# Kernel tuning notes

Measured on AMD Instinct MI355X. Metric: run time of the kernel, lower is better.

The kernel has to match this reference:

```python
import jax, jax.numpy as jnp
import numpy as np

B, L, IN, OUT = 32, 2048, 192, 2
H, N2, NL = 512, 32, 4  # hidden_dim, d_state//2 complex modes, num_layers


def setup_inputs() -> dict:
    key = jax.random.key(0)
    ks = jax.random.split(key, 8)
    neural_input = jax.random.normal(ks[0], (B, L, IN), jnp.float32)
    W_in = jax.random.normal(ks[1], (IN, H), jnp.float32) / np.sqrt(IN)
    b_in = jnp.zeros((H,), jnp.float32)
    # S4D kernel params (stacked over layers)
    log_dt = jax.random.uniform(ks[2], (NL, H), jnp.float32, np.log(1e-3), np.log(1e-1))
    Cri = jax.random.normal(ks[3], (NL, H, N2, 2), jnp.float32)  # complex C as (re, im)
    log_A_real = jnp.full((NL, H, N2), np.log(0.5), jnp.float32)
    A_imag = jnp.broadcast_to(np.pi * jnp.arange(N2, dtype=np.float32), (NL, H, N2)).astype(jnp.float32)
    D = jax.random.normal(ks[4], (NL, H), jnp.float32)
    # position-wise output conv1x1 producing 2H channels for GLU
    conv_w = jax.random.normal(ks[5], (NL, 2 * H, H), jnp.float32) / np.sqrt(H)
    conv_b = jnp.zeros((NL, 2 * H), jnp.float32)
    W_out = jax.random.normal(ks[6], (H, OUT), jnp.float32) / np.sqrt(H)
    b_out = jnp.zeros((OUT,), jnp.float32)
    return dict(neural_input=neural_input, W_in=W_in, b_in=b_in, log_dt=log_dt,
                Cri=Cri, log_A_real=log_A_real, A_imag=A_imag, D=D,
                conv_w=conv_w, conv_b=conv_b, W_out=W_out, b_out=b_out)


def _s4d_layer(u, log_dt, Cri, log_A_real, A_imag, D, conv_w, conv_b):
    # u: (B, H, L)
    Lx = u.shape[-1]
    dt = jnp.exp(log_dt)[:, None]                       # (H, 1)
    C = Cri[..., 0] + 1j * Cri[..., 1]                  # (H, N2) complex
    A = -jnp.exp(log_A_real) + 1j * A_imag              # (H, N2)
    dtA = A * dt                                        # (H, N2)
    Ct = C * (jnp.exp(dtA) - 1.0) / A                   # (H, N2)
    # Vandermonde kernel: K[h, l] = 2 Re sum_n Ct[h,n] exp(dtA[h,n] * l)
    vand = jnp.exp(dtA[..., None] * jnp.arange(Lx))     # (H, N2, L) complex
    K = 2.0 * jnp.einsum('hn,hnl->hl', Ct, vand).real   # (H, L)
    # circular conv via FFT at length 2L (== linear conv, causal)
    k_f = jnp.fft.rfft(K, n=2 * Lx)
    u_f = jnp.fft.rfft(u, n=2 * Lx)
    y = jnp.fft.irfft(u_f * k_f, n=2 * Lx)[..., :Lx]    # (B, H, L)
    y = y + u * D[:, None]
    y = jax.nn.gelu(y, approximate=False)               # torch nn.GELU (erf)
    # conv1x1 to 2H channels + GLU over channel dim
    z = jnp.einsum('oh,bhl->bol', conv_w, y) + conv_b[None, :, None]
    a, b = jnp.split(z, 2, axis=1)
    return a * jax.nn.sigmoid(b)


def reference(neural_input, W_in, b_in, log_dt, Cri, log_A_real, A_imag, D,
              conv_w, conv_b, W_out, b_out):
    x = neural_input @ W_in + b_in          # (B, L, H)
    u = jnp.transpose(x, (0, 2, 1))         # (B, H, L) channels-first for SSM
    for i in range(NL):
        u = _s4d_layer(u, log_dt[i], Cri[i], log_A_real[i], A_imag[i],
                       D[i], conv_w[i], conv_b[i])
    y = jnp.transpose(u, (0, 2, 1))         # (B, L, H)
    return y @ W_out + b_out                # (B, L, OUT)
```

## Files before the change

kernel.cpp:

```cpp
#include <hip/hip_runtime.h>
#include <hip/hip_bf16.h>
#include <math.h>

#define BB 32
#define LL 2048
#define INP 192
#define OUTC 2
#define HH 512
#define NN2 32
#define NNL 4
#define TABB 32768

using short8 = __attribute__((ext_vector_type(8))) short;
using f32x4  = __attribute__((ext_vector_type(4))) float;
using f32x2  = __attribute__((ext_vector_type(2))) float;

__device__ __forceinline__ float sigmoidf_(float x) {
  return 1.0f / (1.0f + expf(-x));
}
__device__ __forceinline__ unsigned short bf16bits(float x) {
  __hip_bfloat16 b = __float2bfloat16(x);
  return __builtin_bit_cast(unsigned short, b);
}
__device__ __forceinline__ float bfval(unsigned short b) {
  unsigned int u = (unsigned int)b << 16;
  return __builtin_bit_cast(float, u);
}
__device__ __forceinline__ float gelu_fast(float x) {
  float s = x * 0.70710678118654752f;
  float ax = fabsf(s);
  float tt = 1.0f / fmaf(0.3275911f, ax, 1.0f);
  float p = fmaf(1.061405429f, tt, -1.453152027f);
  p = fmaf(p, tt, 1.421413741f);
  p = fmaf(p, tt, -0.284496736f);
  p = fmaf(p, tt, 0.254829592f);
  float e = __expf(-s * s);
  float er = 1.0f - p * tt * e;
  er = copysignf(er, s);
  return 0.5f * x * (1.0f + er);
}
__device__ __forceinline__ void gload16(const void* gsrc, void* ldst) {
  __builtin_amdgcn_global_load_lds(
      (const __attribute__((address_space(1))) void*)gsrc,
      (__attribute__((address_space(3))) void*)ldst, 16, 0, 0);
}

__global__ __launch_bounds__(256) void k_params(const float* __restrict__ log_dt,
                                                const float* __restrict__ Cri,
                                                const float* __restrict__ lAr,
                                                const float* __restrict__ Aim,
                                                float* __restrict__ P) {
  int idx = blockIdx.x * 256 + threadIdx.x;
  if (idx >= NNL * HH * NN2) return;
  float dt  = expf(log_dt[idx / NN2]);
  float Are = -expf(lAr[idx]);
  float Aimv = Aim[idx];
  float dre = Are * dt, dim = Aimv * dt;
  float er = expf(dre);
  float wrv = er * cosf(dim);
  float wiv = er * sinf(dim);
  float Er = wrv - 1.0f, Ei = wiv;
  float den = Are * Are + Aimv * Aimv;
  float Fr = (Er * Are + Ei * Aimv) / den;
  float Fi = (Ei * Are - Er * Aimv) / den;
  float Cre = Cri[idx * 2 + 0], Cim = Cri[idx * 2 + 1];
  P[idx * 4 + 0] = wrv;
  P[idx * 4 + 1] = wiv;
  P[idx * 4 + 2] = 2.0f * (Cre * Fr - Cim * Fi);
  P[idx * 4 + 3] = 2.0f * (Cre * Fi + Cim * Fr);
}

__global__ __launch_bounds__(64) void k_tables(const float* __restrict__ P,
                                               char* __restrict__ Tab) {
  __shared__ float kk[32];
  int tid = threadIdx.x;
  int lh = blockIdx.x;
  char* tb = Tab + (size_t)lh * TABB;
  if (tid < 32) {
    int n = tid;
    const float4 pq = reinterpret_cast<const float4*>(P)[(size_t)lh * NN2 + n];
    float wr = pq.x, wi = pq.y, c2r = pq.z, c2i = pq.w;
    int mt = n >> 4;
    float pr = 1.0f, pi = 0.0f;
    for (int d = 0; d < 32; ++d) {
      {
        int t_ = 31 - d;
        int lane = ((t_ >> 3) << 4) + (n & 15);
        int j = t_ & 7;
        unsigned short hr = bf16bits(pr);
        unsigned short lr = bf16bits(pr - bfval(hr));
        unsigned short hi_ = bf16bits(pi);
        unsigned short li_ = bf16bits(pi - bfval(hi_));
        *(unsigned short*)(tb + (mt * 2 + 0) * 1024 + lane * 16 + j * 2) = hr;
        *(unsigned short*)(tb + (mt * 2 + 1) * 1024 + lane * 16 + j * 2) = hi_;
        *(unsigned short*)(tb + 4096 + (mt * 2 + 0) * 1024 + lane * 16 + j * 2) = lr;
        *(unsigned short*)(tb + 4096 + (mt * 2 + 1) * 1024 + lane * 16 + j * 2) = li_;
      }
      {
        int mtT = d >> 4;
        int lane = (((n & 15) >> 2) << 4) + (d & 15);
        int jre = n & 3, jim = (n & 3) + 4;
        unsigned short hr = bf16bits(pr);
        unsigned short lr = bf16bits(pr - bfval(hr));
        float nim = -pi;
        unsigned short hi_ = bf16bits(nim);
        unsigned short li_ = bf16bits(nim - bfval(hi_));
        char* bh = tb + 8192 + (mtT * 2 + mt) * 1024 + lane * 16;
        char* bl = tb + 12288 + (mtT * 2 + mt) * 1024 + lane * 16;
        *(unsigned short*)(bh + jre * 2) = hr;
        *(unsigned short*)(bh + jim * 2) = hi_;
        *(unsigned short*)(bl + jre * 2) = lr;
        *(unsigned short*)(bl + jim * 2) = li_;
      }
      float kp = c2r * pr - c2i * pi;
      #pragma unroll
      for (int k = 1; k < 32; k <<= 1) kp += __shfl_xor(kp, k, 32);
      if (n == 0) kk[d] = kp;
      float nr = pr * wr - pi * wi;
      pi = pr * wi + pi * wr;
      pr = nr;
    }
    float w32r = pr, w32i = pi;
    float c2wr = c2r * wr - c2i * wi;
    float c2wi = c2r * wi + c2i * wr;
    int s = ((n >> 4) << 2) + (n & 3);
    int gg = (n & 15) >> 2;
    float pmr = 1.0f, pmi = 0.0f;
    for (int m = 0; m < 16; ++m) {
      float* q = (float*)(tb + 20480 + (size_t)((s * 64) + (gg * 16 + m)) * 24);
      q[0] = w32r; q[1] = w32i; q[2] = pmr; q[3] = pmi; q[4] = c2wr; q[5] = c2wi;
      float t2 = pmr * w32r - pmi * w32i;
      pmi = pmr * w32i + pmi * w32r;
      pmr = t2;
    }
  }
  __syncthreads();
  for (int idx = tid; idx < 1024; idx += 64) {
    int mt = idx >> 9, rem = idx & 511;
    int lane = rem >> 3, j = rem & 7;
    int tt = (mt << 4) + (lane & 15);
    int jf = ((lane >> 4) << 3) + j;
    float val = (jf <= tt) ? kk[tt - jf] : 0.0f;
    unsigned short hb = bf16bits(val);
    unsigned short lb = bf16bits(val - bfval(hb));
    *(unsigned short*)(tb + 16384 + mt * 1024 + lane * 16 + j * 2) = hb;
    *(unsigned short*)(tb + 18432 + mt * 1024 + lane * 16 + j * 2) = lb;
  }
}

__global__ __launch_bounds__(256) void k_tobf16(const float* __restrict__ src,
                                                __hip_bfloat16* __restrict__ dst,
                                                int n) {
  int i = (blockIdx.x * 256 + threadIdx.x) * 4;
  if (i >= n) return;
  float4 v = *reinterpret_cast<const float4*>(&src[i]);
  dst[i + 0] = __float2bfloat16(v.x);
  dst[i + 1] = __float2bfloat16(v.y);
  dst[i + 2] = __float2bfloat16(v.z);
  dst[i + 3] = __float2bfloat16(v.w);
}

__global__ __launch_bounds__(256) void k_ingemm(const float* __restrict__ X,
                                                const float* __restrict__ W,
                                                const float* __restrict__ bias,
                                                float* __restrict__ U) {
  __shared__ float At[32][132];
  __shared__ float Bt[32][132];
  int lt = blockIdx.x * 128;
  int ht = blockIdx.y * 128;
  int b  = blockIdx.z;
  int tid = threadIdx.x;
  int tr = tid >> 4, tc = tid & 15;
  int r0 = tr * 4, c0 = tc * 4;
  float acc[2][2][4][4] = {};
  for (int kt = 0; kt < INP; kt += 32) {
    for (int i = tid; i < 32 * 128; i += 256) {
      int k = i >> 7, r = i & 127;
      At[k][r] = W[(size_t)(kt + k) * HH + ht + r];
    }
    {
      int k4 = (tid & 7) * 4;
      int cb = tid >> 3;
      #pragma unroll
      for (int p = 0; p < 4; ++p) {
        int c = cb + 32 * p;
        const float4 v = *reinterpret_cast<const float4*>(
            &X[((size_t)b * LL + lt + c) * INP + kt + k4]);
        Bt[k4 + 0][c] = v.x; Bt[k4 + 1][c] = v.y;
        Bt[k4 + 2][c] = v.z; Bt[k4 + 3][c] = v.w;
      }
    }
    __syncthreads();
    #pragma unroll
    for (int k = 0; k < 32; ++k) {
      float4 a0 = *reinterpret_cast<const float4*>(&At[k][r0]);
      float4 a1 = *reinterpret_cast<const float4*>(&At[k][r0 + 64]);
      float4 b0 = *reinterpret_cast<const float4*>(&Bt[k][c0]);
      float4 b1 = *reinterpret_cast<const float4*>(&Bt[k][c0 + 64]);
      float ar[2][4] = {{a0.x, a0.y, a0.z, a0.w}, {a1.x, a1.y, a1.z, a1.w}};
      float bc[2][4] = {{b0.x, b0.y, b0.z, b0.w}, {b1.x, b1.y, b1.z, b1.w}};
      #pragma unroll
      for (int p = 0; p < 2; ++p)
        #pragma unroll
        for (int q = 0; q < 2; ++q)
          #pragma unroll
          for (int i = 0; i < 4; ++i)
            #pragma unroll
            for (int j = 0; j < 4; ++j)
              acc[p][q][i][j] = fmaf(ar[p][i], bc[q][j], acc[p][q][i][j]);
    }
    __syncthreads();
  }
  #pragma unroll
  for (int p = 0; p < 2; ++p)
    #pragma unroll
    for (int i = 0; i < 4; ++i) {
      int h = ht + r0 + p * 64 + i;
      float bv = bias[h];
      #pragma unroll
      for (int q = 0; q < 2; ++q) {
        float4 o;
        o.x = acc[p][q][i][0] + bv;
        o.y = acc[p][q][i][1] + bv;
        o.z = acc[p][q][i][2] + bv;
        o.w = acc[p][q][i][3] + bv;
        *reinterpret_cast<float4*>(&U[((size_t)b * HH + h) * LL + lt + c0 + q * 64]) = o;
      }
    }
}

__global__ __launch_bounds__(256) void k_scan(const float* __restrict__ U,
                                              __hip_bfloat16* __restrict__ Ybf,
                                              const char* __restrict__ Tab,
                                              const float* __restrict__ Dp) {
  int t = threadIdx.x;
  int lane = t & 63;
  int row = __builtin_amdgcn_readfirstlane(blockIdx.x * 4 + (t >> 6));
  int h = row & (HH - 1);
  const char* tb = Tab + (size_t)h * TABB;
  const float* urow = U + (size_t)row * LL;
  int g = lane >> 4, m = lane & 15;

  short8 uh[4], ul[4];
  #pragma unroll
  for (int c0 = 0; c0 < 4; ++c0) {
    const float* p = urow + 512 * c0 + 32 * m + 8 * g;
    float4 va = *reinterpret_cast<const float4*>(p);
    float4 vb = *reinterpret_cast<const float4*>(p + 4);
    float v[8] = {va.x, va.y, va.z, va.w, vb.x, vb.y, vb.z, vb.w};
    short8 hi, lo;
    #pragma unroll
    for (int j = 0; j < 8; ++j) {
      unsigned short hb = bf16bits(v[j]);
      hi[j] = (short)hb;
      lo[j] = (short)bf16bits(v[j] - bfval(hb));
    }
    uh[c0] = hi;
    ul[c0] = lo;
  }

  f32x4 Z[2][2][4];
  #pragma unroll
  for (int mt = 0; mt < 2; ++mt)
    #pragma unroll
    for (int reim = 0; reim < 2; ++reim) {
      short8 whi = *reinterpret_cast<const short8*>(tb + (mt * 2 + reim) * 1024 + lane * 16);
      short8 wlo = *reinterpret_cast<const short8*>(tb + 4096 + (mt * 2 + reim) * 1024 + lane * 16);
      #pragma unroll
      for (int c0 = 0; c0 < 4; ++c0) {
        f32x4 z = {0.f, 0.f, 0.f, 0.f};
        z = __builtin_amdgcn_mfma_f32_16x16x32_bf16(whi, uh[c0], z, 0, 0, 0);
        z = __builtin_amdgcn_mfma_f32_16x16x32_bf16(whi, ul[c0], z, 0, 0, 0);
        z = __builtin_amdgcn_mfma_f32_16x16x32_bf16(wlo, uh[c0], z, 0, 0, 0);
        Z[mt][reim][c0] = z;
      }
    }

  float aR[8][4], aI[8][4];
  #pragma unroll
  for (int s = 0; s < 8; ++s) {
    int mt = s >> 2, i = s & 3;
    const char* plb = tb + 20480 + (size_t)(s * 64 + lane) * 24;
    f32x2 w32 = *reinterpret_cast<const f32x2*>(plb);
    f32x2 w32m = *reinterpret_cast<const f32x2*>(plb + 8);
    f32x2 c2w = *reinterpret_cast<const f32x2*>(plb + 16);
    float r1r = w32[0], r1i = w32[1];
    float r2r = r1r * r1r - r1i * r1i, r2i = 2.f * r1r * r1i;
    float r4r = r2r * r2r - r2i * r2i, r4i = 2.f * r2r * r2i;
    float r8r = r4r * r4r - r4i * r4i, r8i = 2.f * r4r * r4i;
    float w16r = r8r * r8r - r8i * r8i, w16i = 2.f * r8r * r8i;
    float Sr = 0.f, Si = 0.f;
    #pragma unroll
    for (int c0 = 0; c0 < 4; ++c0) {
      float Pr = Z[mt][0][c0][i], Pi = Z[mt][1][c0][i];
      {
        float qr = __shfl_up(Pr, 1u, 16), qi = __shfl_up(Pi, 1u, 16);
        if (m < 1) { qr = 0.f; qi = 0.f; }
        Pr = fmaf(r1r, qr, fmaf(-r1i, qi, Pr));
        Pi = fmaf(r1r, qi, fmaf(r1i, qr, Pi));
      }
      {
        float qr = __shfl_up(Pr, 2u, 16), qi = __shfl_up(Pi, 2u, 16);
        if (m < 2) { qr = 0.f; qi = 0.f; }
        Pr = fmaf(r2r, qr, fmaf(-r2i, qi, Pr));
        Pi = fmaf(r2r, qi, fmaf(r2i, qr, Pi));
      }
      {
        float qr = __shfl_up(Pr, 4u, 16), qi = __shfl_up(Pi, 4u, 16);
        if (m < 4) { qr = 0.f; qi = 0.f; }
        Pr = fmaf(r4r, qr, fmaf(-r4i, qi, Pr));
        Pi = fmaf(r4r, qi, fmaf(r4i, qr, Pi));
      }
      {
        float qr = __shfl_up(Pr, 8u, 16), qi = __shfl_up(Pi, 8u, 16);
        if (m < 8) { qr = 0.f; qi = 0.f; }
        Pr = fmaf(r8r, qr, fmaf(-r8i, qi, Pr));
        Pi = fmaf(r8r, qi, fmaf(r8i, qr, Pi));
      }
      float eqr = __shfl_up(Pr, 1u, 16), eqi = __shfl_up(Pi, 1u, 16);
      if (m == 0) { eqr = 0.f; eqi = 0.f; }
      float Er = fmaf(w32m[0], Sr, fmaf(-w32m[1], Si, eqr));
      float Ei = fmaf(w32m[0], Si, fmaf(w32m[1], Sr, eqi));
      aR[s][c0] = c2w[0] * Er - c2w[1] * Ei;
      aI[s][c0] = c2w[0] * Ei + c2w[1] * Er;
      float lr = __shfl(Pr, 15, 16), li = __shfl(Pi, 15, 16);
      float nS = fmaf(w16r, Sr, fmaf(-w16i, Si, lr));
      Si = fmaf(w16r, Si, fmaf(w16i, Sr, li));
      Sr = nS;
    }
  }

  short8 afh[2][4], afl[2][4];
  #pragma unroll
  for (int kt = 0; kt < 2; ++kt)
    #pragma unroll
    for (int c0 = 0; c0 < 4; ++c0) {
      float av[8] = {aR[kt * 4 + 0][c0], aR[kt * 4 + 1][c0], aR[kt * 4 + 2][c0], aR[kt * 4 + 3][c0],
                     aI[kt * 4 + 0][c0], aI[kt * 4 + 1][c0], aI[kt * 4 + 2][c0], aI[kt * 4 + 3][c0]};
      short8 hi, lo;
      #pragma unroll
      for (int j = 0; j < 8; ++j) {
        unsigned short hb = bf16bits(av[j]);
        hi[j] = (short)hb;
        lo[j] = (short)bf16bits(av[j] - bfval(hb));
      }
      afh[kt][c0] = hi;
      afl[kt][c0] = lo;
    }

  f32x4 y[2][4];
  #pragma unroll
  for (int mtT = 0; mtT < 2; ++mtT) {
    short8 fh = *reinterpret_cast<const short8*>(tb + 16384 + mtT * 1024 + lane * 16);
    short8 fl = *reinterpret_cast<const short8*>(tb + 18432 + mtT * 1024 + lane * 16);
    short8 wch0 = *reinterpret_cast<const short8*>(tb + 8192 + (mtT * 2 + 0) * 1024 + lane * 16);
    short8 wcl0 = *reinterpret_cast<const short8*>(tb + 12288 + (mtT * 2 + 0) * 1024 + lane * 16);
    short8 wch1 = *reinterpret_cast<const short8*>(tb + 8192 + (mtT * 2 + 1) * 1024 + lane * 16);
    short8 wcl1 = *reinterpret_cast<const short8*>(tb + 12288 + (mtT * 2 + 1) * 1024 + lane * 16);
    #pragma unroll
    for (int c0 = 0; c0 < 4; ++c0) {
      f32x4 acc = {0.f, 0.f, 0.f, 0.f};
      acc = __builtin_amdgcn_mfma_f32_16x16x32_bf16(fh, uh[c0], acc, 0, 0, 0);
      acc = __builtin_amdgcn_mfma_f32_16x16x32_bf16(fh, ul[c0], acc, 0, 0, 0);
      acc = __builtin_amdgcn_mfma_f32_16x16x32_bf16(fl, uh[c0], acc, 0, 0, 0);
      acc = __builtin_amdgcn_mfma_f32_16x16x32_bf16(wch0, afh[0][c0], acc, 0, 0, 0);
      acc = __builtin_amdgcn_mfma_f32_16x16x32_bf16(wch0, afl[0][c0], acc, 0, 0, 0);
      acc = __builtin_amdgcn_mfma_f32_16x16x32_bf16(wcl0, afh[0][c0], acc, 0, 0, 0);
      acc = __builtin_amdgcn_mfma_f32_16x16x32_bf16(wch1, afh[1][c0], acc, 0, 0, 0);
      acc = __builtin_amdgcn_mfma_f32_16x16x32_bf16(wch1, afl[1][c0], acc, 0, 0, 0);
      acc = __builtin_amdgcn_mfma_f32_16x16x32_bf16(wcl1, afh[1][c0], acc, 0, 0, 0);
      y[mtT][c0] = acc;
    }
  }

  float Dv = Dp[h];
  #pragma unroll
  for (int mtT = 0; mtT < 2; ++mtT)
    #pragma unroll
    for (int c0 = 0; c0 < 4; ++c0) {
      int eb = 512 * c0 + 32 * m + 16 * mtT + 4 * g;
      float4 uu = *reinterpret_cast<const float4*>(urow + eb);
      f32x4 vv = y[mtT][c0];
      unsigned short b0 = bf16bits(gelu_fast(fmaf(Dv, uu.x, vv[0])));
      unsigned short b1 = bf16bits(gelu_fast(fmaf(Dv, uu.y, vv[1])));
      unsigned short b2 = bf16bits(gelu_fast(fmaf(Dv, uu.z, vv[2])));
      unsigned short b3 = bf16bits(gelu_fast(fmaf(Dv, uu.w, vv[3])));
      uint2 wo;
      wo.x = (unsigned int)b0 | ((unsigned int)b1 << 16);
      wo.y = (unsigned int)b2 | ((unsigned int)b3 << 16);
      *reinterpret_cast<uint2*>(Ybf + (size_t)row * LL + eb) = wo;
    }
}

__global__ __launch_bounds__(256) void k_transpose(const __hip_bfloat16* __restrict__ src,
                                                   __hip_bfloat16* __restrict__ dst) {
  __shared__ short lds[32][132];
  int t = threadIdx.x;
  int l0 = blockIdx.x * 128;
  int h0 = blockIdx.y * 32;
  int b  = blockIdx.z;
  const short* S = (const short*)(src + (size_t)b * HH * LL);
  short* D = (short*)(dst + (size_t)b * LL * HH);
  {
    int h = t >> 3, s0 = (t & 7) * 2;
    #pragma unroll
    for (int s = s0; s < s0 + 2; ++s) {
      float4 v = *reinterpret_cast<const float4*>(&S[(size_t)(h0 + h) * LL + l0 + s * 8]);
      *reinterpret_cast<float2*>(&lds[h][s * 8])     = make_float2(v.x, v.y);
      *reinterpret_cast<float2*>(&lds[h][s * 8 + 4]) = make_float2(v.z, v.w);
    }
  }
  __syncthreads();
  {
    int l = t >> 1, half = t & 1;
    unsigned int w[8];
    #pragma unroll
    for (int j = 0; j < 8; ++j) {
      unsigned short s0 = (unsigned short)lds[half * 16 + 2 * j][l];
      unsigned short s1 = (unsigned short)lds[half * 16 + 2 * j + 1][l];
      w[j] = (unsigned int)s0 | ((unsigned int)s1 << 16);
    }
    uint4* dp = reinterpret_cast<uint4*>(&D[(size_t)(l0 + l) * HH + h0 + half * 16]);
    dp[0] = make_uint4(w[0], w[1], w[2], w[3]);
    dp[1] = make_uint4(w[4], w[5], w[6], w[7]);
  }
}

__global__ __launch_bounds__(256) void k_conv(const __hip_bfloat16* __restrict__ Ytb,
                                              const __hip_bfloat16* __restrict__ CWb,
                                              const float* __restrict__ CB,
                                              float* __restrict__ U) {
  __shared__ short Alds[128 * 64];
  __shared__ short Blds[128 * 64];
  int lt = blockIdx.x * 128;
  int ot = blockIdx.y * 64;
  int b  = blockIdx.z;
  int t = threadIdx.x;
  int wid = t >> 6, lane = t & 63;
  int wr = wid >> 1, wc = wid & 1;
  int l15 = lane & 15, l4 = lane >> 4;
  f32x4 zero = {0.f, 0.f, 0.f, 0.f};
  f32x4 accA[2][4], accG[2][4];
  #pragma unroll
  for (int m = 0; m < 2; ++m)
    #pragma unroll
    for (int n = 0; n < 4; ++n) { accA[m][n] = zero; accG[m][n] = zero; }

  const char* Yb = (const char*)(Ytb + (size_t)b * LL * HH);
  const char* Wb = (const char*)CWb;

  for (int kt = 0; kt < HH; kt += 64) {
    #pragma unroll
    for (int it = 0; it < 4; ++it) {
      int d = 16 * (t + 256 * it);
      int rowl = d >> 7, cb = d & 127;
      int orow = (rowl < 64) ? (ot + rowl) : (448 + ot + rowl);
      gload16(Wb + (size_t)orow * 1024 + kt * 2 + (cb ^ ((rowl & 7) << 4)),
              (char*)Alds + d);
    }
    #pragma unroll
    for (int it = 0; it < 4; ++it) {
      int d = 16 * (t + 256 * it);
      int rowl = d >> 7, cb = d & 127;
      gload16(Yb + ((size_t)(lt + rowl) * 512 + kt) * 2 + (cb ^ ((rowl & 7) << 4)),
              (char*)Blds + d);
    }
    __syncthreads();
    #pragma unroll
    for (int ks = 0; ks < 2; ++ks) {
      short8 af[4], bf[4];
      #pragma unroll
      for (int m = 0; m < 4; ++m) {
        int mrow = ((m < 2) ? (wr * 32 + m * 16) : (64 + wr * 32 + (m - 2) * 16)) + l15;
        int colb = (ks * 64 + 16 * l4) ^ ((mrow & 7) << 4);
        af[m] = *reinterpret_cast<const short8*>((const char*)Alds + mrow * 128 + colb);
      }
      #pragma unroll
      for (int n = 0; n < 4; ++n) {
        int nrow = wc * 64 + n * 16 + l15;
        int colb = (ks * 64 + 16 * l4) ^ ((nrow & 7) << 4);
        bf[n] = *reinterpret_cast<const short8*>((const char*)Blds + nrow * 128 + colb);
      }
      #pragma unroll
      for (int m = 0; m < 2; ++m)
        #pragma unroll
        for (int n = 0; n < 4; ++n) {
          accA[m][n] = __builtin_amdgcn_mfma_f32_16x16x32_bf16(af[m], bf[n], accA[m][n], 0, 0, 0);
          accG[m][n] = __builtin_amdgcn_mfma_f32_16x16x32_bf16(af[m + 2], bf[n], accG[m][n], 0, 0, 0);
        }
    }
    __syncthreads();
  }
  #pragma unroll
  for (int m = 0; m < 2; ++m) {
    #pragma unroll
    for (int r = 0; r < 4; ++r) {
      int rowl = wr * 32 + m * 16 + l4 * 4 + r;
      float ba = CB[ot + rowl];
      float bg = CB[512 + ot + rowl];
      float* urow_ = U + ((size_t)b * HH + ot + rowl) * LL + lt + wc * 64;
      #pragma unroll
      for (int n = 0; n < 4; ++n) {
        float a = accA[m][n][r] + ba;
        float g = accG[m][n][r] + bg;
        urow_[n * 16 + l15] = a * sigmoidf_(g);
      }
    }
  }
}

__global__ __launch_bounds__(256) void k_outgemm(const float* __restrict__ U,
                                                 const float* __restrict__ Wo,
                                                 const float* __restrict__ bo,
                                                 float* __restrict__ out) {
  int bl = blockIdx.x * 256 + threadIdx.x;
  int b = bl >> 11, l = bl & (LL - 1);
  float a0 = 0.0f, a1 = 0.0f;
  const float* up = U + (size_t)b * HH * LL + l;
  #pragma unroll 4
  for (int h = 0; h < HH; ++h) {
    float v = up[(size_t)h * LL];
    a0 = fmaf(v, Wo[h * 2 + 0], a0);
    a1 = fmaf(v, Wo[h * 2 + 1], a1);
  }
  out[(size_t)bl * 2 + 0] = a0 + bo[0];
  out[(size_t)bl * 2 + 1] = a1 + bo[1];
}

extern "C" void kernel_launch(void* const* d_in, const int* in_sizes, int n_in,
                              void* d_out, int out_size, void* d_ws, size_t ws_size,
                              hipStream_t stream) {
  const float* X      = (const float*)d_in[0];
  const float* Win    = (const float*)d_in[1];
  const float* bin    = (const float*)d_in[2];
  const float* log_dt = (const float*)d_in[3];
  const float* Cri    = (const float*)d_in[4];
  const float* lAr    = (const float*)d_in[5];
  const float* Aim    = (const float*)d_in[6];
  const float* Dp     = (const float*)d_in[7];
  const float* CW     = (const float*)d_in[8];
  const float* CB     = (const float*)d_in[9];
  const float* Wo     = (const float*)d_in[10];
  const float* bo     = (const float*)d_in[11];
  float* out = (float*)d_out;

  const size_t Pfloats   = (size_t)NNL * HH * NN2 * 4;
  const size_t CWfloats  = (size_t)NNL * 2 * HH * HH / 2;
  const size_t Tabfloats = (size_t)NNL * HH * (TABB / 4);
  const size_t HL        = (size_t)HH * LL;

  float* P = (float*)d_ws;
  __hip_bfloat16* CWb = (__hip_bfloat16*)(P + Pfloats);
  char* Tab = (char*)(P + Pfloats + CWfloats);
  size_t head = Pfloats + CWfloats + Tabfloats;

  size_t ws_floats = ws_size / sizeof(float);
  size_t avail = (ws_floats > head) ? (ws_floats - head) : 0;
  int G = (int)(avail / (HL + HL / 2));
  if (G > 16) G = 16;
  if (G < 1) G = 1;

  float* U = P + head;
  __hip_bfloat16* Ybf = (__hip_bfloat16*)(U + (size_t)G * HL);
  __hip_bfloat16* Yt  = Ybf + (size_t)G * HL;

  k_params<<<(NNL * HH * NN2 + 255) / 256, 256, 0, stream>>>(log_dt, Cri, lAr, Aim, P);
  k_tables<<<NNL * HH, 64, 0, stream>>>(P, Tab);
  k_tobf16<<<(NNL * 2 * HH * HH) / 1024, 256, 0, stream>>>(CW, CWb, NNL * 2 * HH * HH);

  for (int b0 = 0; b0 < BB; b0 += G) {
    int g = (BB - b0 < G) ? (BB - b0) : G;
    k_ingemm<<<dim3(LL / 128, HH / 128, g), 256, 0, stream>>>(
        X + (size_t)b0 * LL * INP, Win, bin, U);
    for (int layer = 0; layer < NNL; ++layer) {
      k_scan<<<g * (HH / 4), 256, 0, stream>>>(
          U, Ybf,
          Tab + (size_t)layer * HH * TABB,
          Dp + (size_t)layer * HH);
      k_transpose<<<dim3(LL / 128, HH / 32, g), 256, 0, stream>>>(Ybf, Yt);
      k_conv<<<dim3(LL / 128, HH / 64, g), 256, 0, stream>>>(
          Yt, CWb + (size_t)layer * 2 * HH * HH, CB + (size_t)layer * 2 * HH, U);
    }
    k_outgemm<<<g * LL / 256, 256, 0, stream>>>(
        U, Wo, bo, out + (size_t)b0 * LL * OUTC);
  }
}
```

Before: 1.325 ms.

## Move input GEMM to split-bf16 MFMA and allow larger batch groups

Replaces the fp32 SIMT input projection GEMM with a bf16 MFMA kernel that uses a hi/lo split (three MFMAs per tile) to keep near-fp32 accuracy. New prep kernels split X and a transposed W_in into hi/lo bf16 arrays in workspace. The batch group size G can now reach 32 and is rounded to a power of two, which reduces the number of launch iterations. The cost is an extra pass over X and more workspace, which could shrink G.

```diff
diff --git a/kernel.cpp b/kernel.cpp
--- a/kernel.cpp
+++ b/kernel.cpp
@@ -160,73 +160,107 @@
   dst[i + 3] = __float2bfloat16(v.w);
 }
 
-__global__ __launch_bounds__(256) void k_ingemm(const float* __restrict__ X,
-                                                const float* __restrict__ W,
+__global__ __launch_bounds__(256) void k_splitx(const float* __restrict__ src,
+                                                __hip_bfloat16* __restrict__ hi,
+                                                __hip_bfloat16* __restrict__ lo,
+                                                int n) {
+  int i = (blockIdx.x * 256 + threadIdx.x) * 4;
+  if (i >= n) return;
+  float4 v = *reinterpret_cast<const float4*>(&src[i]);
+  float vv[4] = {v.x, v.y, v.z, v.w};
+  unsigned short hb[4], lb[4];
+  #pragma unroll
+  for (int j = 0; j < 4; ++j) {
+    hb[j] = bf16bits(vv[j]);
+    lb[j] = bf16bits(vv[j] - bfval(hb[j]));
+  }
+  *reinterpret_cast<uint2*>(hi + i) = make_uint2(
+      (unsigned)hb[0] | ((unsigned)hb[1] << 16), (unsigned)hb[2] | ((unsigned)hb[3] << 16));
+  *reinterpret_cast<uint2*>(lo + i) = make_uint2(
+      (unsigned)lb[0] | ((unsigned)lb[1] << 16), (unsigned)lb[2] | ((unsigned)lb[3] << 16));
+}
+
+__global__ __launch_bounds__(256) void k_prepwt(const float* __restrict__ W,
+                                                __hip_bfloat16* __restrict__ hi,
+                                                __hip_bfloat16* __restrict__ lo) {
+  int idx = blockIdx.x * 256 + threadIdx.x;
+  if (idx >= HH * INP) return;
+  int h = idx / INP, k = idx - h * INP;
+  float v = W[(size_t)k * HH + h];
+  unsigned short hb = bf16bits(v);
+  hi[idx] = __builtin_bit_cast(__hip_bfloat16, hb);
+  lo[idx] = __float2bfloat16(v - bfval(hb));
+}
+
+__global__ __launch_bounds__(256) void k_ingemm(const __hip_bfloat16* __restrict__ Xhi,
+                                                const __hip_bfloat16* __restrict__ Xlo,
+                                                const __hip_bfloat16* __restrict__ Wthi,
+                                                const __hip_bfloat16* __restrict__ Wtlo,
                                                 const float* __restrict__ bias,
                                                 float* __restrict__ U) {
-  __shared__ float At[32][132];
-  __shared__ float Bt[32][132];
   int lt = blockIdx.x * 128;
   int ht = blockIdx.y * 128;
   int b  = blockIdx.z;
-  int tid = threadIdx.x;
-  int tr = tid >> 4, tc = tid & 15;
-  int r0 = tr * 4, c0 = tc * 4;
-  float acc[2][2][4][4] = {};
-  for (int kt = 0; kt < INP; kt += 32) {
-    for (int i = tid; i < 32 * 128; i += 256) {
-      int k = i >> 7, r = i & 127;
-      At[k][r] = W[(size_t)(kt + k) * HH + ht + r];
-    }
-    {
-      int k4 = (tid & 7) * 4;
-      int cb = tid >> 3;
-      #pragma unroll
-      for (int p = 0; p < 4; ++p) {
-        int c = cb + 32 * p;
-        const float4 v = *reinterpret_cast<const float4*>(
-            &X[((size_t)b * LL + lt + c) * INP + kt + k4]);
-        Bt[k4 + 0][c] = v.x; Bt[k4 + 1][c] = v.y;
-        Bt[k4 + 2][c] = v.z; Bt[k4 + 3][c] = v.w;
-      }
-    }
-    __syncthreads();
-    #pragma unroll
-    for (int k = 0; k < 32; ++k) {
-      float4 a0 = *reinterpret_cast<const float4*>(&At[k][r0]);
-      float4 a1 = *reinterpret_cast<const float4*>(&At[k][r0 + 64]);
-      float4 b0 = *reinterpret_cast<const float4*>(&Bt[k][c0]);
-      float4 b1 = *reinterpret_cast<const float4*>(&Bt[k][c0 + 64]);
-      float ar[2][4] = {{a0.x, a0.y, a0.z, a0.w}, {a1.x, a1.y, a1.z, a1.w}};
-      float bc[2][4] = {{b0.x, b0.y, b0.z, b0.w}, {b1.x, b1.y, b1.z, b1.w}};
-      #pragma unroll
-      for (int p = 0; p < 2; ++p)
-        #pragma unroll
-        for (int q = 0; q < 2; ++q)
-          #pragma unroll
-          for (int i = 0; i < 4; ++i)
-            #pragma unroll
-            for (int j = 0; j < 4; ++j)
-              acc[p][q][i][j] = fmaf(ar[p][i], bc[q][j], acc[p][q][i][j]);
-    }
-    __syncthreads();
-  }
-  #pragma unroll
-  for (int p = 0; p < 2; ++p)
-    #pragma unroll
-    for (int i = 0; i < 4; ++i) {
-      int h = ht + r0 + p * 64 + i;
-      float bv = bias[h];
-      #pragma unroll
-      for (int q = 0; q < 2; ++q) {
-        float4 o;
-        o.x = acc[p][q][i][0] + bv;
-        o.y = acc[p][q][i][1] + bv;
-        o.z = acc[p][q][i][2] + bv;
-        o.w = acc[p][q][i][3] + bv;
-        *reinterpret_cast<float4*>(&U[((size_t)b * HH + h) * LL + lt + c0 + q * 64]) = o;
-      }
-    }
+  int t = threadIdx.x;
+  int wid = t >> 6, lane = t & 63;
+  int wrow = wid >> 1, wcol = wid & 1;
+  int l15 = lane & 15, g = lane >> 4;
+
+  const short* Xh = (const short*)Xhi + (size_t)b * LL * INP;
+  const short* Xl = (const short*)Xlo + (size_t)b * LL * INP;
+  const short* Bh = (const short*)Wthi;
+  const short* Bl = (const short*)Wtlo;
+
+  f32x4 acc[4][4];
+  #pragma unroll
+  for (int m = 0; m < 4; ++m)
+    #pragma unroll
+    for (int n = 0; n < 4; ++n) acc[m][n] = f32x4{0.f, 0.f, 0.f, 0.f};
+
+  int lbase = lt + wrow * 64 + l15;
+  int hbase = ht + wcol * 64 + l15;
+
+  #pragma unroll
+  for (int ks = 0; ks < 6; ++ks) {
+    int k0 = ks * 32 + 8 * g;
+    short8 ah[4], al[4], bh[4], bl[4];
+    #pragma unroll
+    for (int m = 0; m < 4; ++m) {
+      size_t off = (size_t)(lbase + m * 16) * INP + k0;
+      ah[m] = *reinterpret_cast<const short8*>(Xh + off);
+      al[m] = *reinterpret_cast<const short8*>(Xl + off);
+    }
+    #pragma unroll
+    for (int n = 0; n < 4; ++n) {
+      size_t off = (size_t)(hbase + n * 16) * INP + k0;
+      bh[n] = *reinterpret_cast<const short8*>(Bh + off);
+      bl[n] = *reinterpret_cast<const short8*>(Bl + off);
+    }
+    #pragma unroll
+    for (int m = 0; m < 4; ++m)
+      #pragma unroll
+      for (int n = 0; n < 4; ++n) {
+        acc[m][n] = __builtin_amdgcn_mfma_f32_16x16x32_bf16(ah[m], bh[n], acc[m][n], 0, 0, 0);
+        acc[m][n] = __builtin_amdgcn_mfma_f32_16x16x32_bf16(ah[m], bl[n], acc[m][n], 0, 0, 0);
+        acc[m][n] = __builtin_amdgcn_mfma_f32_16x16x32_bf16(al[m], bh[n], acc[m][n], 0, 0, 0);
+      }
+  }
+
+  #pragma unroll
+  for (int n = 0; n < 4; ++n) {
+    int h = hbase + n * 16;
+    float bv = bias[h];
+    #pragma unroll
+    for (int m = 0; m < 4; ++m) {
+      int l0 = lt + wrow * 64 + m * 16 + g * 4;
+      float4 o;
+      o.x = acc[m][n][0] + bv;
+      o.y = acc[m][n][1] + bv;
+      o.z = acc[m][n][2] + bv;
+      o.w = acc[m][n][3] + bv;
+      *reinterpret_cast<float4*>(&U[((size_t)b * HH + h) * LL + l0]) = o;
+    }
+  }
 }
 
 __global__ __launch_bounds__(256) void k_scan(const float* __restrict__ U,
@@ -547,18 +581,28 @@
   const size_t Pfloats   = (size_t)NNL * HH * NN2 * 4;
   const size_t CWfloats  = (size_t)NNL * 2 * HH * HH / 2;
   const size_t Tabfloats = (size_t)NNL * HH * (TABB / 4);
+  const size_t Wtfloats  = (size_t)HH * INP;
+  const size_t Xnf       = (size_t)BB * LL * INP;
   const size_t HL        = (size_t)HH * LL;
 
   float* P = (float*)d_ws;
   __hip_bfloat16* CWb = (__hip_bfloat16*)(P + Pfloats);
   char* Tab = (char*)(P + Pfloats + CWfloats);
-  size_t head = Pfloats + CWfloats + Tabfloats;
+  __hip_bfloat16* Wthi = (__hip_bfloat16*)(P + Pfloats + CWfloats + Tabfloats);
+  __hip_bfloat16* Wtlo = Wthi + Wtfloats;
+  __hip_bfloat16* Xhi  = (__hip_bfloat16*)(P + Pfloats + CWfloats + Tabfloats + Wtfloats);
+  __hip_bfloat16* Xlo  = Xhi + Xnf;
+  size_t head = Pfloats + CWfloats + Tabfloats + Wtfloats + Xnf;
 
   size_t ws_floats = ws_size / sizeof(float);
   size_t avail = (ws_floats > head) ? (ws_floats - head) : 0;
   int G = (int)(avail / (HL + HL / 2));
-  if (G > 16) G = 16;
-  if (G < 1) G = 1;
+  if (G >= 32) G = 32;
+  else if (G >= 16) G = 16;
+  else if (G >= 8) G = 8;
+  else if (G >= 4) G = 4;
+  else if (G >= 2) G = 2;
+  else G = 1;
 
   float* U = P + head;
   __hip_bfloat16* Ybf = (__hip_bfloat16*)(U + (size_t)G * HL);
@@ -567,11 +611,13 @@
   k_params<<<(NNL * HH * NN2 + 255) / 256, 256, 0, stream>>>(log_dt, Cri, lAr, Aim, P);
   k_tables<<<NNL * HH, 64, 0, stream>>>(P, Tab);
   k_tobf16<<<(NNL * 2 * HH * HH) / 1024, 256, 0, stream>>>(CW, CWb, NNL * 2 * HH * HH);
+  k_prepwt<<<(HH * INP + 255) / 256, 256, 0, stream>>>(Win, Wthi, Wtlo);
+  k_splitx<<<(int)(Xnf / 1024), 256, 0, stream>>>(X, Xhi, Xlo, (int)Xnf);
 
   for (int b0 = 0; b0 < BB; b0 += G) {
     int g = (BB - b0 < G) ? (BB - b0) : G;
     k_ingemm<<<dim3(LL / 128, HH / 128, g), 256, 0, stream>>>(
-        X + (size_t)b0 * LL * INP, Win, bin, U);
+        Xhi + (size_t)b0 * LL * INP, Xlo + (size_t)b0 * LL * INP, Wthi, Wtlo, bin, U);
     for (int layer = 0; layer < NNL; ++layer) {
       k_scan<<<g * (HH / 4), 256, 0, stream>>>(
           U, Ybf,
```

Result: faster. 1.290 ms (-2.7%).
